# Kernel optimization log

Measured on AMD Instinct MI355X. Metric: run time of the kernel, lower is better.

## Reference

```python
import jax, jax.numpy as jnp
import numpy as np

N = 8192      # num_nodes
B = 16        # batch
IN_DIM = 2    # input_dim
HID = 64      # hid_dim
K = 2         # diffusion_steps
DEG = 16
E = N * DEG
F = IN_DIM + HID            # concat(input, state) feature dim
NUM_MAT = 2 * K + 1         # dual random walk: 2 matrices * K steps + identity


def _spmm(vals, rows, cols, x):
    # sparse [N,N] @ dense [N,M]: y[rows[e]] += vals[e] * x[cols[e]]
    return jax.ops.segment_sum(vals[:, None] * x[cols], rows, num_segments=N)


def _diff_conv(x, W, b, edge_src, edge_dst, vals1, vals2):
    # x: [B, N, F] -> [B, N*out_dim]; Chebyshev-like diffusion recursion
    x0 = jnp.transpose(x, (1, 2, 0)).reshape(N, F * B)  # [N, F*B]
    xs = [x0]
    # matrix 1 = D_out^-1 A (edges src->dst), matrix 2 = D_in^-1 A^T (edges dst->src)
    for rows, cols, vals in ((edge_src, edge_dst, vals1), (edge_dst, edge_src, vals2)):
        x1 = _spmm(vals, rows, cols, x0)
        xs.append(x1)
        xp, xc = x0, x1
        for _ in range(2, K + 1):
            xn = 2.0 * _spmm(vals, rows, cols, xc) - xp
            xs.append(xn)
            xp, xc = xc, xn
    xstk = jnp.stack(xs, 0).reshape(NUM_MAT, N, F, B)
    xstk = jnp.transpose(xstk, (3, 1, 2, 0)).reshape(B * N, F * NUM_MAT)
    out = xstk @ W + b  # [B*N, out_dim]
    return out.reshape(B, -1)


def setup_inputs() -> dict:
    key = jax.random.key(0)
    k = jax.random.split(key, 8)
    inputs = jax.random.normal(k[0], (B, N * IN_DIM), jnp.float32)
    state = jax.random.normal(k[1], (B, N * HID), jnp.float32)
    edge_src = jax.random.randint(k[2], (E,), 0, N)
    edge_dst = jax.random.randint(k[3], (E,), 0, N)
    a = jax.random.uniform(k[4], (E,), jnp.float32) + 0.1  # positive edge weights
    dout = jax.ops.segment_sum(a, edge_src, num_segments=N)
    din = jax.ops.segment_sum(a, edge_dst, num_segments=N)
    vals1 = a / jnp.where(dout > 0, dout, 1.0)[edge_src]  # random-walk normalize A
    vals2 = a / jnp.where(din > 0, din, 1.0)[edge_dst]    # random-walk normalize A^T
    std_g = 1.414 * np.sqrt(2.0 / (F * NUM_MAT + 2 * HID)).astype(np.float32)
    std_c = 1.414 * np.sqrt(2.0 / (F * NUM_MAT + HID)).astype(np.float32)
    W_gate = jax.random.normal(k[5], (F * NUM_MAT, 2 * HID), jnp.float32) * std_g
    b_gate = jnp.zeros((2 * HID,), jnp.float32)
    W_cand = jax.random.normal(k[6], (F * NUM_MAT, HID), jnp.float32) * std_c
    b_cand = jnp.zeros((HID,), jnp.float32)
    return dict(inputs=inputs, state=state, edge_src=edge_src, edge_dst=edge_dst,
                vals1=vals1, vals2=vals2, W_gate=W_gate, b_gate=b_gate,
                W_cand=W_cand, b_cand=b_cand)


def reference(inputs, state, edge_src, edge_dst, vals1, vals2,
              W_gate, b_gate, W_cand, b_cand):
    i = inputs.reshape(B, N, IN_DIM)
    s = state.reshape(B, N, HID)
    x = jnp.concatenate([i, s], axis=2)  # [B, N, F]
    value = jax.nn.sigmoid(_diff_conv(x, W_gate, b_gate, edge_src, edge_dst, vals1, vals2))
    value = value.reshape(B, N, 2 * HID)
    r = value[..., :HID].reshape(B, N * HID)
    u = value[..., HID:].reshape(B, N * HID)
    rs = (r * state).reshape(B, N, HID)
    xc = jnp.concatenate([i, rs], axis=2)
    c = jnp.tanh(_diff_conv(xc, W_cand, b_cand, edge_src, edge_dst, vals1, vals2))
    new_state = u * state + (1.0 - u) * c
    return (new_state, new_state)
```

## Files before the change

### kernel.cpp

```cpp
#include <hip/hip_runtime.h>
#include <cstddef>
#include <cstdint>

#define NNODES 8192
#define BATCH  16
#define FDIM   66
#define HID    64
#define CCH    1056
#define NEDGE  131072
#define NFB    8650752
#define SN     524288
#define OUTHALF 8388608
#define KPAD   352
#define LDA    360
#define GN     8

typedef __attribute__((ext_vector_type(8))) short bf16x8;
typedef __attribute__((ext_vector_type(4))) float f32x4;

static __device__ __forceinline__ float bf2f(ushort u) {
    union { uint32_t i; float f; } c; c.i = ((uint32_t)u) << 16; return c.f;
}
static __device__ __forceinline__ ushort f2bf(float f) {
    union { float f; uint32_t i; } c; c.f = f;
    uint32_t lsb = (c.i >> 16) & 1;
    return (ushort)((c.i + 0x7fffu + lsb) >> 16);
}


__global__ void zero_counts_kernel(int* __restrict__ c1, int* __restrict__ c2) {
    int i = blockIdx.x * 256 + threadIdx.x;
    if (i < NNODES) { c1[i] = 0; c2[i] = 0; }
}

__global__ void hist_kernel(const int* __restrict__ src, const int* __restrict__ dst,
                            int* __restrict__ c1, int* __restrict__ c2) {
    int e = blockIdx.x * 256 + threadIdx.x;
    if (e < NEDGE) {
        atomicAdd(&c1[src[e]], 1);
        atomicAdd(&c2[dst[e]], 1);
    }
}

__global__ __launch_bounds__(1024) void scan_kernel(const int* __restrict__ counts,
                                                    int* __restrict__ rowptr,
                                                    int* __restrict__ cursor) {
    __shared__ int sh[1024];
    int tid = threadIdx.x;
    int base = tid * 8;
    int local[8];
    int sum = 0;
#pragma unroll
    for (int j = 0; j < 8; ++j) { local[j] = counts[base + j]; sum += local[j]; }
    sh[tid] = sum;
    __syncthreads();
    for (int off = 1; off < 1024; off <<= 1) {
        int v = (tid >= off) ? sh[tid - off] : 0;
        __syncthreads();
        sh[tid] += v;
        __syncthreads();
    }
    int p = sh[tid] - sum;
#pragma unroll
    for (int j = 0; j < 8; ++j) {
        cursor[base + j] = p;
        p += local[j];
        rowptr[base + j + 1] = p;
    }
    if (tid == 0) rowptr[0] = 0;
}

__global__ void scatter_kernel(const int* __restrict__ src, const int* __restrict__ dst,
                               const float* __restrict__ v1, const float* __restrict__ v2,
                               int* __restrict__ cur1, int* __restrict__ cur2,
                               int* __restrict__ cols1, float* __restrict__ valsC1,
                               int* __restrict__ cols2, float* __restrict__ valsC2) {
    int e = blockIdx.x * 256 + threadIdx.x;
    if (e < NEDGE) {
        int r1 = src[e];
        int p1 = atomicAdd(&cur1[r1], 1);
        cols1[p1] = dst[e];
        valsC1[p1] = v1[e];
        int r2 = dst[e];
        int p2 = atomicAdd(&cur2[r2], 1);
        cols2[p2] = src[e];
        valsC2[p2] = v2[e];
    }
}


__global__ void convert_w_kernel(const float* __restrict__ Wg, const float* __restrict__ Wc,
                                 ushort* __restrict__ WgT, ushort* __restrict__ WcT) {
    int i = blockIdx.x * 256 + threadIdx.x;
    if (i >= 192 * KPAD) return;
    int col = i / KPAD, kk = i - col * KPAD;
    if (col < 128) {
        WgT[col * KPAD + kk] = (kk < 330) ? f2bf(Wg[kk * 128 + col]) : (ushort)0;
    } else {
        int c = col - 128;
        WcT[c * KPAD + kk] = (kk < 330) ? f2bf(Wc[kk * 64 + c]) : (ushort)0;
    }
}


__global__ void build_x0_kernel(const float* __restrict__ inputs, const float* __restrict__ state,
                                ushort* __restrict__ X0) {
    int idx = blockIdx.x * 256 + threadIdx.x;
    if (idx >= NFB) return;
    int b = idx & 15;
    int t = idx >> 4;
    int f = t % FDIM;
    int n = t / FDIM;
    float v;
    if (f < 2) v = inputs[(size_t)b * (NNODES * 2) + n * 2 + f];
    else       v = state[(size_t)b * SN + n * HID + (f - 2)];
    X0[idx] = f2bf(v);
}


static __device__ __forceinline__ void fma8(float* acc, uint4 d, float v) {
    acc[0] += v * bf2f((ushort)(d.x));  acc[1] += v * bf2f((ushort)(d.x >> 16));
    acc[2] += v * bf2f((ushort)(d.y));  acc[3] += v * bf2f((ushort)(d.y >> 16));
    acc[4] += v * bf2f((ushort)(d.z));  acc[5] += v * bf2f((ushort)(d.z >> 16));
    acc[6] += v * bf2f((ushort)(d.w));  acc[7] += v * bf2f((ushort)(d.w >> 16));
}

static __device__ __forceinline__ uint4 blend_pack8(const float* acc, uint4 p,
                                                    float alpha, float beta) {
    float o[8];
    o[0] = alpha * acc[0] + beta * bf2f((ushort)(p.x));
    o[1] = alpha * acc[1] + beta * bf2f((ushort)(p.x >> 16));
    o[2] = alpha * acc[2] + beta * bf2f((ushort)(p.y));
    o[3] = alpha * acc[3] + beta * bf2f((ushort)(p.y >> 16));
    o[4] = alpha * acc[4] + beta * bf2f((ushort)(p.z));
    o[5] = alpha * acc[5] + beta * bf2f((ushort)(p.z >> 16));
    o[6] = alpha * acc[6] + beta * bf2f((ushort)(p.w));
    o[7] = alpha * acc[7] + beta * bf2f((ushort)(p.w >> 16));
    uint4 r;
    r.x = (uint32_t)f2bf(o[0]) | ((uint32_t)f2bf(o[1]) << 16);
    r.y = (uint32_t)f2bf(o[2]) | ((uint32_t)f2bf(o[3]) << 16);
    r.z = (uint32_t)f2bf(o[4]) | ((uint32_t)f2bf(o[5]) << 16);
    r.w = (uint32_t)f2bf(o[6]) | ((uint32_t)f2bf(o[7]) << 16);
    return r;
}

__global__ __launch_bounds__(128) void spmm_kernel(const int* __restrict__ rowptr,
                                                   const int* __restrict__ cols,
                                                   const float* __restrict__ vals,
                                                   const ushort* __restrict__ x,
                                                   const ushort* __restrict__ xp,
                                                   ushort* __restrict__ y,
                                                   float alpha, float beta) {
    int n = blockIdx.x;
    int t = threadIdx.x;
    int s = rowptr[n], e = rowptr[n + 1];
    float a0[8] = {0, 0, 0, 0, 0, 0, 0, 0};
    float a1[8] = {0, 0, 0, 0, 0, 0, 0, 0};
    bool tail = t < 4;
    for (int i = s; i < e; ++i) {
        float v = vals[i];
        int c = cols[i];
        const uint4* xb = (const uint4*)(x + (size_t)c * CCH);
        fma8(a0, xb[t], v);
        if (tail) fma8(a1, xb[128 + t], v);
    }
    uint4* yb = (uint4*)(y + (size_t)n * CCH);
    const uint4* xpb = (const uint4*)(xp + (size_t)n * CCH);
    uint4 p0 = (beta != 0.f) ? xpb[t] : make_uint4(0, 0, 0, 0);
    yb[t] = blend_pack8(a0, p0, alpha, beta);
    if (tail) {
        uint4 p1 = (beta != 0.f) ? xpb[128 + t] : make_uint4(0, 0, 0, 0);
        yb[128 + t] = blend_pack8(a1, p1, alpha, beta);
    }
}


__global__ __launch_bounds__(256) void gate_mfma(const ushort* __restrict__ Xb,
                                                 const ushort* __restrict__ WgT,
                                                 const float* __restrict__ bg,
                                                 const float* __restrict__ state,
                                                 float* __restrict__ U,
                                                 ushort* __restrict__ X0mut) {
    __shared__ __align__(16) ushort At[16 * LDA];
    int tid = threadIdx.x;
    int wave = tid >> 6, lane = tid & 63;
    int row = lane & 15, quad = lane >> 4;
    int c0 = (wave * 2) * 16 + row;
    int c1 = (wave * 2 + 1) * 16 + row;

    bf16x8 w0[11], w1[11];
#pragma unroll
    for (int k = 0; k < 11; ++k) {
        w0[k] = *(const bf16x8*)(WgT + (size_t)c0 * KPAD + k * 32 + quad * 8);
        w1[k] = *(const bf16x8*)(WgT + (size_t)c1 * KPAD + k * 32 + quad * 8);
    }
    float bias0 = bg[c0], bias1 = bg[c1];

    for (int p = tid; p < 16 * 22; p += 256) {
        int b = p / 22, kk = 330 + p % 22;
        At[b * LDA + kk] = 0;
    }

    int nodeBase = blockIdx.x * GN;
    for (int g = 0; g < GN; ++g) {
        int n = nodeBase + g;
        __syncthreads();
        for (int p = tid; p < 2640; p += 256) {
            int m = p / 528;
            int r2 = p - m * 528;
            int f = r2 >> 3;
            int bp = r2 & 7;
            uint d = *(const uint*)(Xb + (size_t)m * NFB + (size_t)n * CCH + f * 16 + bp * 2);
            int kk = f * 5 + m;
            int b = bp * 2;
            At[b * LDA + kk] = (ushort)d;
            At[(b + 1) * LDA + kk] = (ushort)(d >> 16);
        }
        __syncthreads();

        f32x4 acc0 = {0.f, 0.f, 0.f, 0.f};
        f32x4 acc1 = {0.f, 0.f, 0.f, 0.f};
#pragma unroll
        for (int k = 0; k < 11; ++k) {
            bf16x8 av = *(const bf16x8*)(At + row * LDA + k * 32 + quad * 8);
            acc0 = __builtin_amdgcn_mfma_f32_16x16x32_bf16(av, w0[k], acc0, 0, 0, 0);
            acc1 = __builtin_amdgcn_mfma_f32_16x16x32_bf16(av, w1[k], acc1, 0, 0, 0);
        }
#pragma unroll
        for (int r = 0; r < 4; ++r) {
            int b = quad * 4 + r;
            float v0 = 1.f / (1.f + __expf(-(acc0[r] + bias0)));
            float v1 = 1.f / (1.f + __expf(-(acc1[r] + bias1)));
            if (wave < 2) {
                float s0 = state[(size_t)b * SN + n * HID + c0];
                float s1 = state[(size_t)b * SN + n * HID + c1];
                X0mut[(size_t)n * CCH + (2 + c0) * 16 + b] = f2bf(v0 * s0);
                X0mut[(size_t)n * CCH + (2 + c1) * 16 + b] = f2bf(v1 * s1);
            } else {
                U[(size_t)b * SN + n * HID + (c0 - HID)] = v0;
                U[(size_t)b * SN + n * HID + (c1 - HID)] = v1;
            }
        }
    }
}


__global__ __launch_bounds__(256) void cand_mfma(const ushort* __restrict__ Xb,
                                                 const ushort* __restrict__ WcT,
                                                 const float* __restrict__ bc,
                                                 const float* __restrict__ state,
                                                 const float* __restrict__ U,
                                                 float* __restrict__ out) {
    __shared__ __align__(16) ushort At[16 * LDA];
    int tid = threadIdx.x;
    int wave = tid >> 6, lane = tid & 63;
    int row = lane & 15, quad = lane >> 4;
    int c = wave * 16 + row;

    bf16x8 w[11];
#pragma unroll
    for (int k = 0; k < 11; ++k)
        w[k] = *(const bf16x8*)(WcT + (size_t)c * KPAD + k * 32 + quad * 8);
    float bias = bc[c];

    for (int p = tid; p < 16 * 22; p += 256) {
        int b = p / 22, kk = 330 + p % 22;
        At[b * LDA + kk] = 0;
    }

    int nodeBase = blockIdx.x * GN;
    for (int g = 0; g < GN; ++g) {
        int n = nodeBase + g;
        __syncthreads();
        for (int p = tid; p < 2640; p += 256) {
            int m = p / 528;
            int r2 = p - m * 528;
            int f = r2 >> 3;
            int bp = r2 & 7;
            uint d = *(const uint*)(Xb + (size_t)m * NFB + (size_t)n * CCH + f * 16 + bp * 2);
            int kk = f * 5 + m;
            int b = bp * 2;
            At[b * LDA + kk] = (ushort)d;
            At[(b + 1) * LDA + kk] = (ushort)(d >> 16);
        }
        __syncthreads();

        f32x4 acc = {0.f, 0.f, 0.f, 0.f};
#pragma unroll
        for (int k = 0; k < 11; ++k) {
            bf16x8 av = *(const bf16x8*)(At + row * LDA + k * 32 + quad * 8);
            acc = __builtin_amdgcn_mfma_f32_16x16x32_bf16(av, w[k], acc, 0, 0, 0);
        }
#pragma unroll
        for (int r = 0; r < 4; ++r) {
            int b = quad * 4 + r;
            float pre = acc[r] + bias;
            float cv = 1.f - 2.f / (__expf(2.f * pre) + 1.f);
            size_t idx = (size_t)b * SN + n * HID + c;
            float uv = U[idx];
            float s = state[idx];
            float ns = uv * s + (1.f - uv) * cv;
            out[idx] = ns;
            out[OUTHALF + idx] = ns;
        }
    }
}


extern "C" void kernel_launch(void* const* d_in, const int* in_sizes, int n_in,
                              void* d_out, int out_size, void* d_ws, size_t ws_size,
                              hipStream_t stream) {
    const float* inputs = (const float*)d_in[0];
    const float* state  = (const float*)d_in[1];
    const int*   esrc   = (const int*)d_in[2];
    const int*   edst   = (const int*)d_in[3];
    const float* v1     = (const float*)d_in[4];
    const float* v2     = (const float*)d_in[5];
    const float* Wg     = (const float*)d_in[6];
    const float* bg     = (const float*)d_in[7];
    const float* Wc     = (const float*)d_in[8];
    const float* bc     = (const float*)d_in[9];
    float* out = (float*)d_out;

    char* ws = (char*)d_ws;
    size_t off = 0;
    auto alloc = [&](size_t bytes) -> void* {
        void* p = ws + off;
        off += (bytes + 255) & ~(size_t)255;
        return p;
    };
    ushort* Xb     = (ushort*)alloc((size_t)5 * NFB * 2);
    float*  U      = (float*)alloc((size_t)OUTHALF * 4);
    ushort* WgT    = (ushort*)alloc((size_t)128 * KPAD * 2);
    ushort* WcT    = (ushort*)alloc((size_t)64 * KPAD * 2);
    int*   counts1 = (int*)alloc(NNODES * 4);
    int*   counts2 = (int*)alloc(NNODES * 4);
    int*   rowptr1 = (int*)alloc((NNODES + 1) * 4);
    int*   rowptr2 = (int*)alloc((NNODES + 1) * 4);
    int*   cursor1 = (int*)alloc(NNODES * 4);
    int*   cursor2 = (int*)alloc(NNODES * 4);
    int*   cols1   = (int*)alloc(NEDGE * 4);
    int*   cols2   = (int*)alloc(NEDGE * 4);
    float* valsC1  = (float*)alloc(NEDGE * 4);
    float* valsC2  = (float*)alloc(NEDGE * 4);

    ushort* X0 = Xb;
    ushort* X1 = Xb + (size_t)1 * NFB;
    ushort* X2 = Xb + (size_t)2 * NFB;
    ushort* X3 = Xb + (size_t)3 * NFB;
    ushort* X4 = Xb + (size_t)4 * NFB;

    zero_counts_kernel<<<(NNODES + 255) / 256, 256, 0, stream>>>(counts1, counts2);
    hist_kernel<<<(NEDGE + 255) / 256, 256, 0, stream>>>(esrc, edst, counts1, counts2);
    scan_kernel<<<1, 1024, 0, stream>>>(counts1, rowptr1, cursor1);
    scan_kernel<<<1, 1024, 0, stream>>>(counts2, rowptr2, cursor2);
    scatter_kernel<<<(NEDGE + 255) / 256, 256, 0, stream>>>(esrc, edst, v1, v2,
                                                            cursor1, cursor2,
                                                            cols1, valsC1, cols2, valsC2);

    convert_w_kernel<<<(192 * KPAD + 255) / 256, 256, 0, stream>>>(Wg, Wc, WgT, WcT);
    build_x0_kernel<<<(NFB + 255) / 256, 256, 0, stream>>>(inputs, state, X0);

    spmm_kernel<<<NNODES, 128, 0, stream>>>(rowptr1, cols1, valsC1, X0, X0, X1, 1.f, 0.f);
    spmm_kernel<<<NNODES, 128, 0, stream>>>(rowptr1, cols1, valsC1, X1, X0, X2, 2.f, -1.f);
    spmm_kernel<<<NNODES, 128, 0, stream>>>(rowptr2, cols2, valsC2, X0, X0, X3, 1.f, 0.f);
    spmm_kernel<<<NNODES, 128, 0, stream>>>(rowptr2, cols2, valsC2, X3, X0, X4, 2.f, -1.f);

    gate_mfma<<<NNODES / GN, 256, 0, stream>>>(Xb, WgT, bg, state, U, X0);

    spmm_kernel<<<NNODES, 128, 0, stream>>>(rowptr1, cols1, valsC1, X0, X0, X1, 1.f, 0.f);
    spmm_kernel<<<NNODES, 128, 0, stream>>>(rowptr1, cols1, valsC1, X1, X0, X2, 2.f, -1.f);
    spmm_kernel<<<NNODES, 128, 0, stream>>>(rowptr2, cols2, valsC2, X0, X0, X3, 1.f, 0.f);
    spmm_kernel<<<NNODES, 128, 0, stream>>>(rowptr2, cols2, valsC2, X3, X0, X4, 2.f, -1.f);

    cand_mfma<<<NNODES / GN, 256, 0, stream>>>(Xb, WcT, bc, state, U, out);
}
```

Baseline: 632.7 us.

## Interleave diffusion slices per (node,batch) row so MFMA reads A directly

Replaces the five separate [N, F*B] bf16 buffers with one interleaved buffer where each (node, batch) row holds all five diffusion slices (72-element padded slices, 384-element row). The gate and candidate MFMA kernels can then load A fragments straight from global memory, with no LDS transpose or barriers, and the weights are permuted to match. SpMM now stages edge indices and values through wave shuffles and unrolls four neighbours at a time for more memory-level parallelism. The cost is strided, padded gathers in SpMM (more bytes per row, including padding), plus one extra zero-padded K step in the MFMA.

```diff
diff --git a/kernel.cpp b/kernel.cpp
--- a/kernel.cpp
+++ b/kernel.cpp
@@ -4,15 +4,13 @@
 
 #define NNODES 8192
 #define BATCH  16
-#define FDIM   66
 #define HID    64
-#define CCH    1056
 #define NEDGE  131072
-#define NFB    8650752
 #define SN     524288
 #define OUTHALF 8388608
-#define KPAD   352
-#define LDA    360
+#define ROWE   384
+#define SLICE  72
+#define NBROW  6144
 #define GN     8
 
 typedef __attribute__((ext_vector_type(8))) short bf16x8;
@@ -92,29 +90,43 @@
 __global__ void convert_w_kernel(const float* __restrict__ Wg, const float* __restrict__ Wc,
                                  ushort* __restrict__ WgT, ushort* __restrict__ WcT) {
     int i = blockIdx.x * 256 + threadIdx.x;
-    if (i >= 192 * KPAD) return;
-    int col = i / KPAD, kk = i - col * KPAD;
+    if (i >= 192 * ROWE) return;
+    int col = i / ROWE, kk = i - col * ROWE;
+    int m = kk / SLICE, f = kk - m * SLICE;
+    bool real = (m < 5) && (f < 66);
     if (col < 128) {
-        WgT[col * KPAD + kk] = (kk < 330) ? f2bf(Wg[kk * 128 + col]) : (ushort)0;
+        WgT[col * ROWE + kk] = real ? f2bf(Wg[(f * 5 + m) * 128 + col]) : (ushort)0;
     } else {
         int c = col - 128;
-        WcT[c * KPAD + kk] = (kk < 330) ? f2bf(Wc[kk * 64 + c]) : (ushort)0;
-    }
-}
-
-
-__global__ void build_x0_kernel(const float* __restrict__ inputs, const float* __restrict__ state,
-                                ushort* __restrict__ X0) {
-    int idx = blockIdx.x * 256 + threadIdx.x;
-    if (idx >= NFB) return;
-    int b = idx & 15;
-    int t = idx >> 4;
-    int f = t % FDIM;
-    int n = t / FDIM;
-    float v;
-    if (f < 2) v = inputs[(size_t)b * (NNODES * 2) + n * 2 + f];
-    else       v = state[(size_t)b * SN + n * HID + (f - 2)];
-    X0[idx] = f2bf(v);
+        WcT[c * ROWE + kk] = real ? f2bf(Wc[(f * 5 + m) * 64 + c]) : (ushort)0;
+    }
+}
+
+
+__global__ void init_x0_kernel(const float* __restrict__ inputs, const float* __restrict__ state,
+                               ushort* __restrict__ x_all) {
+    int i = blockIdx.x * 256 + threadIdx.x;
+    if (i >= NNODES * 16 * 12) return;
+    int nb = i / 12, p = i - nb * 12;
+    int n = nb >> 4, b = nb & 15;
+    if (p >= 9) {
+        *(uint4*)(x_all + (size_t)nb * ROWE + 360 + (p - 9) * 8) = make_uint4(0, 0, 0, 0);
+        return;
+    }
+    float v[8];
+#pragma unroll
+    for (int k = 0; k < 8; ++k) {
+        int e = 8 * p + k;
+        if (e < 2)       v[k] = inputs[b * (NNODES * 2) + n * 2 + e];
+        else if (e < 66) v[k] = state[(size_t)b * SN + n * HID + (e - 2)];
+        else             v[k] = 0.f;
+    }
+    uint4 r;
+    r.x = (uint32_t)f2bf(v[0]) | ((uint32_t)f2bf(v[1]) << 16);
+    r.y = (uint32_t)f2bf(v[2]) | ((uint32_t)f2bf(v[3]) << 16);
+    r.z = (uint32_t)f2bf(v[4]) | ((uint32_t)f2bf(v[5]) << 16);
+    r.w = (uint32_t)f2bf(v[6]) | ((uint32_t)f2bf(v[7]) << 16);
+    *(uint4*)(x_all + (size_t)nb * ROWE + 8 * p) = r;
 }
 
 
@@ -147,84 +159,101 @@
 __global__ __launch_bounds__(128) void spmm_kernel(const int* __restrict__ rowptr,
                                                    const int* __restrict__ cols,
                                                    const float* __restrict__ vals,
-                                                   const ushort* __restrict__ x,
+                                                   const ushort* __restrict__ xin,
                                                    const ushort* __restrict__ xp,
-                                                   ushort* __restrict__ y,
+                                                   ushort* __restrict__ yout,
                                                    float alpha, float beta) {
     int n = blockIdx.x;
     int t = threadIdx.x;
+    int lane = t & 63;
+    int b0 = t / 9, j0 = t - b0 * 9;
+    int p1 = 128 + t;
+    int b1 = p1 / 9, j1 = p1 - b1 * 9;
+    int off0 = b0 * ROWE + j0 * 8;
+    int off1 = b1 * ROWE + j1 * 8;
+    bool tail = t < 16;
+
     int s = rowptr[n], e = rowptr[n + 1];
     float a0[8] = {0, 0, 0, 0, 0, 0, 0, 0};
     float a1[8] = {0, 0, 0, 0, 0, 0, 0, 0};
-    bool tail = t < 4;
-    for (int i = s; i < e; ++i) {
-        float v = vals[i];
-        int c = cols[i];
-        const uint4* xb = (const uint4*)(x + (size_t)c * CCH);
-        fma8(a0, xb[t], v);
-        if (tail) fma8(a1, xb[128 + t], v);
-    }
-    uint4* yb = (uint4*)(y + (size_t)n * CCH);
-    const uint4* xpb = (const uint4*)(xp + (size_t)n * CCH);
-    uint4 p0 = (beta != 0.f) ? xpb[t] : make_uint4(0, 0, 0, 0);
-    yb[t] = blend_pack8(a0, p0, alpha, beta);
+
+    for (int base = s; base < e; base += 64) {
+        int rem = e - base;
+        if (rem > 64) rem = 64;
+        int mc = 0; float mv = 0.f;
+        if (lane < rem) { mc = cols[base + lane]; mv = vals[base + lane]; }
+        for (int j = 0; j < rem; j += 4) {
+            int   c0 = __shfl(mc, j);
+            float v0 = __shfl(mv, j);
+            int   c1 = __shfl(mc, (j + 1) & 63);
+            float v1 = (j + 1 < rem) ? __shfl(mv, (j + 1) & 63) : 0.f;
+            int   c2 = __shfl(mc, (j + 2) & 63);
+            float v2 = (j + 2 < rem) ? __shfl(mv, (j + 2) & 63) : 0.f;
+            int   c3 = __shfl(mc, (j + 3) & 63);
+            float v3 = (j + 3 < rem) ? __shfl(mv, (j + 3) & 63) : 0.f;
+            const ushort* s0 = xin + (size_t)c0 * NBROW;
+            const ushort* s1 = xin + (size_t)c1 * NBROW;
+            const ushort* s2 = xin + (size_t)c2 * NBROW;
+            const ushort* s3 = xin + (size_t)c3 * NBROW;
+            uint4 d0 = *(const uint4*)(s0 + off0);
+            uint4 d1 = *(const uint4*)(s1 + off0);
+            uint4 d2 = *(const uint4*)(s2 + off0);
+            uint4 d3 = *(const uint4*)(s3 + off0);
+            fma8(a0, d0, v0); fma8(a0, d1, v1); fma8(a0, d2, v2); fma8(a0, d3, v3);
+            if (tail) {
+                uint4 e0 = *(const uint4*)(s0 + off1);
+                uint4 e1 = *(const uint4*)(s1 + off1);
+                uint4 e2 = *(const uint4*)(s2 + off1);
+                uint4 e3 = *(const uint4*)(s3 + off1);
+                fma8(a1, e0, v0); fma8(a1, e1, v1); fma8(a1, e2, v2); fma8(a1, e3, v3);
+            }
+        }
+    }
+    const ushort* xpr = xp + (size_t)n * NBROW;
+    ushort* yr = yout + (size_t)n * NBROW;
+    uint4 pp0 = (beta != 0.f) ? *(const uint4*)(xpr + off0) : make_uint4(0, 0, 0, 0);
+    *(uint4*)(yr + off0) = blend_pack8(a0, pp0, alpha, beta);
     if (tail) {
-        uint4 p1 = (beta != 0.f) ? xpb[128 + t] : make_uint4(0, 0, 0, 0);
-        yb[128 + t] = blend_pack8(a1, p1, alpha, beta);
-    }
-}
-
-
-__global__ __launch_bounds__(256) void gate_mfma(const ushort* __restrict__ Xb,
+        uint4 pp1 = (beta != 0.f) ? *(const uint4*)(xpr + off1) : make_uint4(0, 0, 0, 0);
+        *(uint4*)(yr + off1) = blend_pack8(a1, pp1, alpha, beta);
+    }
+}
+
+
+__global__ __launch_bounds__(256) void gate_mfma(const ushort* __restrict__ x_all,
                                                  const ushort* __restrict__ WgT,
                                                  const float* __restrict__ bg,
                                                  const float* __restrict__ state,
                                                  float* __restrict__ U,
-                                                 ushort* __restrict__ X0mut) {
-    __shared__ __align__(16) ushort At[16 * LDA];
+                                                 ushort* __restrict__ x_mut) {
     int tid = threadIdx.x;
     int wave = tid >> 6, lane = tid & 63;
     int row = lane & 15, quad = lane >> 4;
-    int c0 = (wave * 2) * 16 + row;
-    int c1 = (wave * 2 + 1) * 16 + row;
-
-    bf16x8 w0[11], w1[11];
-#pragma unroll
-    for (int k = 0; k < 11; ++k) {
-        w0[k] = *(const bf16x8*)(WgT + (size_t)c0 * KPAD + k * 32 + quad * 8);
-        w1[k] = *(const bf16x8*)(WgT + (size_t)c1 * KPAD + k * 32 + quad * 8);
+    int c0 = wave * 32 + row;
+    int c1 = c0 + 16;
+
+    bf16x8 w0[12], w1[12];
+#pragma unroll
+    for (int k = 0; k < 12; ++k) {
+        w0[k] = *(const bf16x8*)(WgT + (size_t)c0 * ROWE + k * 32 + quad * 8);
+        w1[k] = *(const bf16x8*)(WgT + (size_t)c1 * ROWE + k * 32 + quad * 8);
     }
     float bias0 = bg[c0], bias1 = bg[c1];
-
-    for (int p = tid; p < 16 * 22; p += 256) {
-        int b = p / 22, kk = 330 + p % 22;
-        At[b * LDA + kk] = 0;
-    }
 
     int nodeBase = blockIdx.x * GN;
     for (int g = 0; g < GN; ++g) {
         int n = nodeBase + g;
-        __syncthreads();
-        for (int p = tid; p < 2640; p += 256) {
-            int m = p / 528;
-            int r2 = p - m * 528;
-            int f = r2 >> 3;
-            int bp = r2 & 7;
-            uint d = *(const uint*)(Xb + (size_t)m * NFB + (size_t)n * CCH + f * 16 + bp * 2);
-            int kk = f * 5 + m;
-            int b = bp * 2;
-            At[b * LDA + kk] = (ushort)d;
-            At[(b + 1) * LDA + kk] = (ushort)(d >> 16);
-        }
-        __syncthreads();
+        const ushort* Ab = x_all + ((size_t)n * 16 + row) * ROWE + quad * 8;
+        bf16x8 a[12];
+#pragma unroll
+        for (int k = 0; k < 12; ++k) a[k] = *(const bf16x8*)(Ab + k * 32);
 
         f32x4 acc0 = {0.f, 0.f, 0.f, 0.f};
         f32x4 acc1 = {0.f, 0.f, 0.f, 0.f};
 #pragma unroll
-        for (int k = 0; k < 11; ++k) {
-            bf16x8 av = *(const bf16x8*)(At + row * LDA + k * 32 + quad * 8);
-            acc0 = __builtin_amdgcn_mfma_f32_16x16x32_bf16(av, w0[k], acc0, 0, 0, 0);
-            acc1 = __builtin_amdgcn_mfma_f32_16x16x32_bf16(av, w1[k], acc1, 0, 0, 0);
+        for (int k = 0; k < 12; ++k) {
+            acc0 = __builtin_amdgcn_mfma_f32_16x16x32_bf16(a[k], w0[k], acc0, 0, 0, 0);
+            acc1 = __builtin_amdgcn_mfma_f32_16x16x32_bf16(a[k], w1[k], acc1, 0, 0, 0);
         }
 #pragma unroll
         for (int r = 0; r < 4; ++r) {
@@ -234,8 +263,8 @@
             if (wave < 2) {
                 float s0 = state[(size_t)b * SN + n * HID + c0];
                 float s1 = state[(size_t)b * SN + n * HID + c1];
-                X0mut[(size_t)n * CCH + (2 + c0) * 16 + b] = f2bf(v0 * s0);
-                X0mut[(size_t)n * CCH + (2 + c1) * 16 + b] = f2bf(v1 * s1);
+                x_mut[((size_t)n * 16 + b) * ROWE + 2 + c0] = f2bf(v0 * s0);
+                x_mut[((size_t)n * 16 + b) * ROWE + 2 + c1] = f2bf(v1 * s1);
             } else {
                 U[(size_t)b * SN + n * HID + (c0 - HID)] = v0;
                 U[(size_t)b * SN + n * HID + (c1 - HID)] = v1;
@@ -245,52 +274,36 @@
 }
 
 
-__global__ __launch_bounds__(256) void cand_mfma(const ushort* __restrict__ Xb,
+__global__ __launch_bounds__(256) void cand_mfma(const ushort* __restrict__ x_all,
                                                  const ushort* __restrict__ WcT,
                                                  const float* __restrict__ bc,
                                                  const float* __restrict__ state,
                                                  const float* __restrict__ U,
                                                  float* __restrict__ out) {
-    __shared__ __align__(16) ushort At[16 * LDA];
     int tid = threadIdx.x;
     int wave = tid >> 6, lane = tid & 63;
     int row = lane & 15, quad = lane >> 4;
     int c = wave * 16 + row;
 
-    bf16x8 w[11];
-#pragma unroll
-    for (int k = 0; k < 11; ++k)
-        w[k] = *(const bf16x8*)(WcT + (size_t)c * KPAD + k * 32 + quad * 8);
+    bf16x8 w[12];
+#pragma unroll
+    for (int k = 0; k < 12; ++k)
+        w[k] = *(const bf16x8*)(WcT + (size_t)c * ROWE + k * 32 + quad * 8);
     float bias = bc[c];
-
-    for (int p = tid; p < 16 * 22; p += 256) {
-        int b = p / 22, kk = 330 + p % 22;
-        At[b * LDA + kk] = 0;
-    }
 
     int nodeBase = blockIdx.x * GN;
     for (int g = 0; g < GN; ++g) {
         int n = nodeBase + g;
-        __syncthreads();
-        for (int p = tid; p < 2640; p += 256) {
-            int m = p / 528;
-            int r2 = p - m * 528;
-            int f = r2 >> 3;
-            int bp = r2 & 7;
-            uint d = *(const uint*)(Xb + (size_t)m * NFB + (size_t)n * CCH + f * 16 + bp * 2);
-            int kk = f * 5 + m;
-            int b = bp * 2;
-            At[b * LDA + kk] = (ushort)d;
-            At[(b + 1) * LDA + kk] = (ushort)(d >> 16);
-        }
-        __syncthreads();
+        const ushort* Ab = x_all + ((size_t)n * 16 + row) * ROWE + quad * 8;
+        bf16x8 a[12];
+#pragma unroll
+        for (int k = 0; k < 12; ++k) a[k] = *(const bf16x8*)(Ab + k * 32);
 
         f32x4 acc = {0.f, 0.f, 0.f, 0.f};
 #pragma unroll
-        for (int k = 0; k < 11; ++k) {
-            bf16x8 av = *(const bf16x8*)(At + row * LDA + k * 32 + quad * 8);
-            acc = __builtin_amdgcn_mfma_f32_16x16x32_bf16(av, w[k], acc, 0, 0, 0);
-        }
+        for (int k = 0; k < 12; ++k)
+            acc = __builtin_amdgcn_mfma_f32_16x16x32_bf16(a[k], w[k], acc, 0, 0, 0);
+
 #pragma unroll
         for (int r = 0; r < 4; ++r) {
             int b = quad * 4 + r;
@@ -329,10 +342,10 @@
         off += (bytes + 255) & ~(size_t)255;
         return p;
     };
-    ushort* Xb     = (ushort*)alloc((size_t)5 * NFB * 2);
+    ushort* x_all  = (ushort*)alloc((size_t)NNODES * NBROW * 2);
     float*  U      = (float*)alloc((size_t)OUTHALF * 4);
-    ushort* WgT    = (ushort*)alloc((size_t)128 * KPAD * 2);
-    ushort* WcT    = (ushort*)alloc((size_t)64 * KPAD * 2);
+    ushort* WgT    = (ushort*)alloc((size_t)128 * ROWE * 2);
+    ushort* WcT    = (ushort*)alloc((size_t)64 * ROWE * 2);
     int*   counts1 = (int*)alloc(NNODES * 4);
     int*   counts2 = (int*)alloc(NNODES * 4);
     int*   rowptr1 = (int*)alloc((NNODES + 1) * 4);
@@ -344,11 +357,11 @@
     float* valsC1  = (float*)alloc(NEDGE * 4);
     float* valsC2  = (float*)alloc(NEDGE * 4);
 
-    ushort* X0 = Xb;
-    ushort* X1 = Xb + (size_t)1 * NFB;
-    ushort* X2 = Xb + (size_t)2 * NFB;
-    ushort* X3 = Xb + (size_t)3 * NFB;
-    ushort* X4 = Xb + (size_t)4 * NFB;
+    ushort* S0 = x_all;
+    ushort* S1 = x_all + 1 * SLICE;
+    ushort* S2 = x_all + 2 * SLICE;
+    ushort* S3 = x_all + 3 * SLICE;
+    ushort* S4 = x_all + 4 * SLICE;
 
     zero_counts_kernel<<<(NNODES + 255) / 256, 256, 0, stream>>>(counts1, counts2);
     hist_kernel<<<(NEDGE + 255) / 256, 256, 0, stream>>>(esrc, edst, counts1, counts2);
@@ -358,20 +371,20 @@
                                                             cursor1, cursor2,
                                                             cols1, valsC1, cols2, valsC2);
 
-    convert_w_kernel<<<(192 * KPAD + 255) / 256, 256, 0, stream>>>(Wg, Wc, WgT, WcT);
-    build_x0_kernel<<<(NFB + 255) / 256, 256, 0, stream>>>(inputs, state, X0);
-
-    spmm_kernel<<<NNODES, 128, 0, stream>>>(rowptr1, cols1, valsC1, X0, X0, X1, 1.f, 0.f);
-    spmm_kernel<<<NNODES, 128, 0, stream>>>(rowptr1, cols1, valsC1, X1, X0, X2, 2.f, -1.f);
-    spmm_kernel<<<NNODES, 128, 0, stream>>>(rowptr2, cols2, valsC2, X0, X0, X3, 1.f, 0.f);
-    spmm_kernel<<<NNODES, 128, 0, stream>>>(rowptr2, cols2, valsC2, X3, X0, X4, 2.f, -1.f);
-
-    gate_mfma<<<NNODES / GN, 256, 0, stream>>>(Xb, WgT, bg, state, U, X0);
-
-    spmm_kernel<<<NNODES, 128, 0, stream>>>(rowptr1, cols1, valsC1, X0, X0, X1, 1.f, 0.f);
-    spmm_kernel<<<NNODES, 128, 0, stream>>>(rowptr1, cols1, valsC1, X1, X0, X2, 2.f, -1.f);
-    spmm_kernel<<<NNODES, 128, 0, stream>>>(rowptr2, cols2, valsC2, X0, X0, X3, 1.f, 0.f);
-    spmm_kernel<<<NNODES, 128, 0, stream>>>(rowptr2, cols2, valsC2, X3, X0, X4, 2.f, -1.f);
-
-    cand_mfma<<<NNODES / GN, 256, 0, stream>>>(Xb, WcT, bc, state, U, out);
-}
+    convert_w_kernel<<<(192 * ROWE + 255) / 256, 256, 0, stream>>>(Wg, Wc, WgT, WcT);
+    init_x0_kernel<<<(NNODES * 16 * 12 + 255) / 256, 256, 0, stream>>>(inputs, state, x_all);
+
+    spmm_kernel<<<NNODES, 128, 0, stream>>>(rowptr1, cols1, valsC1, S0, S0, S1, 1.f, 0.f);
+    spmm_kernel<<<NNODES, 128, 0, stream>>>(rowptr1, cols1, valsC1, S1, S0, S2, 2.f, -1.f);
+    spmm_kernel<<<NNODES, 128, 0, stream>>>(rowptr2, cols2, valsC2, S0, S0, S3, 1.f, 0.f);
+    spmm_kernel<<<NNODES, 128, 0, stream>>>(rowptr2, cols2, valsC2, S3, S0, S4, 2.f, -1.f);
+
+    gate_mfma<<<NNODES / GN, 256, 0, stream>>>(x_all, WgT, bg, state, U, x_all);
+
+    spmm_kernel<<<NNODES, 128, 0, stream>>>(rowptr1, cols1, valsC1, S0, S0, S1, 1.f, 0.f);
+    spmm_kernel<<<NNODES, 128, 0, stream>>>(rowptr1, cols1, valsC1, S1, S0, S2, 2.f, -1.f);
+    spmm_kernel<<<NNODES, 128, 0, stream>>>(rowptr2, cols2, valsC2, S0, S0, S3, 1.f, 0.f);
+    spmm_kernel<<<NNODES, 128, 0, stream>>>(rowptr2, cols2, valsC2, S3, S0, S4, 2.f, -1.f);
+
+    cand_mfma<<<NNODES / GN, 256, 0, stream>>>(x_all, WcT, bc, state, U, out);
+}
```

New measurement: 967.6 us. 52.9% more time.
